# Performance work log

Measured on AMD Instinct MI355X. Metric: run time of the kernel, lower is better.

Reference implementation:

```python
import jax, jax.numpy as jnp
import numpy as np

STATE_DIM = 512
N_AGENTS = 16
N_ACTIONS = 32
EMBED = 512          # mixing_embed_dim
Q_IN = STATE_DIM + N_AGENTS * N_ACTIONS  # 1024 (coma_critic arch)
ROWS = 32768         # bs * ts = 64 * 512


def _linear_params(key, d_in, d_out):
    kw, kb = jax.random.split(key)
    bound = 1.0 / np.sqrt(d_in)
    W = jax.random.uniform(kw, (d_in, d_out), minval=-bound, maxval=bound, dtype=jnp.float32)
    b = jax.random.uniform(kb, (d_out,), minval=-bound, maxval=bound, dtype=jnp.float32)
    return W, b


def setup_inputs() -> dict:
    key = jax.random.key(0)
    ks = jax.random.split(key, 8)
    states = jax.random.normal(ks[0], (ROWS, STATE_DIM), dtype=jnp.float32)
    actions = jax.random.uniform(ks[1], (ROWS, N_AGENTS * N_ACTIONS), dtype=jnp.float32)
    Qw1, Qb1 = _linear_params(ks[2], Q_IN, EMBED)
    Qw2, Qb2 = _linear_params(ks[3], EMBED, EMBED)
    Qw3, Qb3 = _linear_params(ks[4], EMBED, 1)
    Vw1, Vb1 = _linear_params(ks[5], STATE_DIM, EMBED)
    Vw2, Vb2 = _linear_params(ks[6], EMBED, EMBED)
    Vw3, Vb3 = _linear_params(ks[7], EMBED, 1)
    return {
        "states": states, "actions": actions,
        "Qw1": Qw1, "Qb1": Qb1, "Qw2": Qw2, "Qb2": Qb2, "Qw3": Qw3, "Qb3": Qb3,
        "Vw1": Vw1, "Vb1": Vb1, "Vw2": Vw2, "Vb2": Vb2, "Vw3": Vw3, "Vb3": Vb3,
    }


def _mlp3(x, W1, b1, W2, b2, W3, b3):
    h = jax.nn.relu(x @ W1 + b1)
    h = jax.nn.relu(h @ W2 + b2)
    return h @ W3 + b3


def reference(states, actions,
              Qw1, Qb1, Qw2, Qb2, Qw3, Qb3,
              Vw1, Vb1, Vw2, Vb2, Vw3, Vb3):
    # coma_critic arch: inputs = cat([states, joint-action one-hots], dim=1)
    inputs = jnp.concatenate([states, actions], axis=1)  # [bs*ts, Q_IN]
    q_outputs = _mlp3(inputs, Qw1, Qb1, Qw2, Qb2, Qw3, Qb3)  # [bs*ts, 1]
    v_outputs = _mlp3(states, Vw1, Vb1, Vw2, Vb2, Vw3, Vb3)  # [bs*ts, 1]
    return q_outputs, v_outputs
```

## Files before the change

kernel.cpp:

```cpp
#include <hip/hip_runtime.h>


#define ROWS 32768
#define EMBED 512

using frag_ab = __attribute__((ext_vector_type(8))) short;
using f32x4   = __attribute__((ext_vector_type(4))) float;

__device__ __forceinline__ unsigned short f2bf(float f) {
    unsigned int u = __builtin_bit_cast(unsigned int, f);
    return (unsigned short)((u + 0x7fffu + ((u >> 16) & 1u)) >> 16);
}

__device__ __forceinline__ void async_copy16(const void* g, void* l) {
    __builtin_amdgcn_global_load_lds(
        (const __attribute__((address_space(1))) unsigned int*)g,
        (__attribute__((address_space(3))) unsigned int*)l, 16, 0, 0);
}

__global__ void init_out(float* __restrict__ out,
                         const float* __restrict__ qb3,
                         const float* __restrict__ vb3) {
    int i = blockIdx.x * 256 + threadIdx.x;
    out[i] = (i < ROWS) ? qb3[0] : vb3[0];
}

__global__ void convert_x(const float* __restrict__ states,
                          const float* __restrict__ actions,
                          unsigned short* __restrict__ X) {
    size_t t = (size_t)blockIdx.x * 256 + threadIdx.x;
    int m   = (int)(t >> 7);
    int col = (int)(t & 127) * 8;
    const float* src = (col < 512) ? states + (size_t)m * 512 + col
                                   : actions + (size_t)m * 512 + (col - 512);
    float4 a = *(const float4*)src;
    float4 b = *(const float4*)(src + 4);
    uint4 o;
    o.x = (unsigned)f2bf(a.x) | ((unsigned)f2bf(a.y) << 16);
    o.y = (unsigned)f2bf(a.z) | ((unsigned)f2bf(a.w) << 16);
    o.z = (unsigned)f2bf(b.x) | ((unsigned)f2bf(b.y) << 16);
    o.w = (unsigned)f2bf(b.z) | ((unsigned)f2bf(b.w) << 16);
    *(uint4*)(X + (size_t)m * 1024 + col) = o;
}

__global__ void prep_w(const float* __restrict__ Qw1, const float* __restrict__ Qw2,
                       const float* __restrict__ Vw1, const float* __restrict__ Vw2,
                       unsigned short* __restrict__ Qw1t, unsigned short* __restrict__ Qw2t,
                       unsigned short* __restrict__ Vw1t, unsigned short* __restrict__ Vw2t) {
    int t = blockIdx.x * 256 + threadIdx.x;
    if (t < 512 * 1024) {
        int n = t >> 10, k = t & 1023;
        Qw1t[t] = f2bf(Qw1[(size_t)k * 512 + n]);
    } else {
        t -= 512 * 1024;
        int seg = t >> 18;
        int r = t & 0x3ffff;
        int n = r >> 9, k = r & 511;
        const float* W = (seg == 0) ? Qw2 : (seg == 1) ? Vw1 : Vw2;
        unsigned short* O = (seg == 0) ? Qw2t : (seg == 1) ? Vw1t : Vw2t;
        O[r] = f2bf(W[(size_t)k * 512 + n]);
    }
}

template <bool FUSE>
__global__ __launch_bounds__(256, 2)
void gemm_bt(const unsigned short* __restrict__ A, int lda,
             const unsigned short* __restrict__ Wt, int K,
             const float* __restrict__ bias,
             unsigned short* __restrict__ H,
             const float* __restrict__ w3, float* __restrict__ out) {
    __shared__ __align__(16) unsigned short As[128 * 32];
    __shared__ __align__(16) unsigned short Bs[128 * 32];

    const int tid  = threadIdx.x;
    const int wave = tid >> 6, lane = tid & 63;
    const int bm = blockIdx.x * 128, bn = blockIdx.y * 128;
    const int wm = (wave & 1) * 64, wn = (wave >> 1) * 64;
    const int lrow = lane & 15, quad = lane >> 4;

    f32x4 acc[4][4] = {};

    const int lin  = wave * 1024 + lane * 16;
    const int rowS = lin >> 6;
    const int colS = (lin & 63) >> 1;

    const unsigned short* gA0 = A  + (size_t)(bm + rowS)      * lda + colS;
    const unsigned short* gA1 = A  + (size_t)(bm + rowS + 64) * lda + colS;
    const unsigned short* gB0 = Wt + (size_t)(bn + rowS)      * K   + colS;
    const unsigned short* gB1 = Wt + (size_t)(bn + rowS + 64) * K   + colS;
    unsigned short* ldsA0 = As + wave * 512;
    unsigned short* ldsA1 = As + 2048 + wave * 512;
    unsigned short* ldsB0 = Bs + wave * 512;
    unsigned short* ldsB1 = Bs + 2048 + wave * 512;

    for (int k0 = 0; k0 < K; k0 += 32) {
        async_copy16(gA0, ldsA0);
        async_copy16(gA1, ldsA1);
        async_copy16(gB0, ldsB0);
        async_copy16(gB1, ldsB1);
        gA0 += 32; gA1 += 32; gB0 += 32; gB1 += 32;
        __syncthreads();

        frag_ab af[4], bfr[4];
#pragma unroll
        for (int i = 0; i < 4; i++)
            af[i] = *(const frag_ab*)&As[(wm + i * 16 + lrow) * 32 + quad * 8];
#pragma unroll
        for (int j = 0; j < 4; j++)
            bfr[j] = *(const frag_ab*)&Bs[(wn + j * 16 + lrow) * 32 + quad * 8];
#pragma unroll
        for (int i = 0; i < 4; i++)
#pragma unroll
            for (int j = 0; j < 4; j++)
                acc[i][j] = __builtin_amdgcn_mfma_f32_16x16x32_bf16(
                    af[i], bfr[j], acc[i][j], 0, 0, 0);
        __syncthreads();
    }

    if (!FUSE) {
#pragma unroll
        for (int j = 0; j < 4; j++) {
            const int col = bn + wn + j * 16 + lrow;
            const float bc = bias[col];
#pragma unroll
            for (int i = 0; i < 4; i++) {
                const int row0 = bm + wm + i * 16 + quad * 4;
#pragma unroll
                for (int r = 0; r < 4; r++) {
                    float v = acc[i][j][r] + bc;
                    v = v > 0.0f ? v : 0.0f;
                    H[(size_t)(row0 + r) * EMBED + col] = f2bf(v);
                }
            }
        }
    } else {
        float bc[4], wc[4];
#pragma unroll
        for (int j = 0; j < 4; j++) {
            const int col = bn + wn + j * 16 + lrow;
            bc[j] = bias[col];
            wc[j] = w3[col];
        }
#pragma unroll
        for (int i = 0; i < 4; i++) {
#pragma unroll
            for (int r = 0; r < 4; r++) {
                float s = 0.0f;
#pragma unroll
                for (int j = 0; j < 4; j++) {
                    float v = acc[i][j][r] + bc[j];
                    v = v > 0.0f ? v : 0.0f;
                    s += v * wc[j];
                }
#pragma unroll
                for (int m = 1; m < 16; m <<= 1) s += __shfl_xor(s, m, 64);
                if (lrow == 0)
                    atomicAdd(&out[bm + wm + i * 16 + quad * 4 + r], s);
            }
        }
    }
}

extern "C" void kernel_launch(void* const* d_in, const int* in_sizes, int n_in,
                              void* d_out, int out_size, void* d_ws, size_t ws_size,
                              hipStream_t stream) {
    const float* states  = (const float*)d_in[0];
    const float* actions = (const float*)d_in[1];
    const float* Qw1 = (const float*)d_in[2];
    const float* Qb1 = (const float*)d_in[3];
    const float* Qw2 = (const float*)d_in[4];
    const float* Qb2 = (const float*)d_in[5];
    const float* Qw3 = (const float*)d_in[6];
    const float* Qb3 = (const float*)d_in[7];
    const float* Vw1 = (const float*)d_in[8];
    const float* Vb1 = (const float*)d_in[9];
    const float* Vw2 = (const float*)d_in[10];
    const float* Vb2 = (const float*)d_in[11];
    const float* Vw3 = (const float*)d_in[12];
    const float* Vb3 = (const float*)d_in[13];
    float* out = (float*)d_out;

    char* ws = (char*)d_ws;
    unsigned short* X    = (unsigned short*)ws;
    unsigned short* h1Q  = (unsigned short*)(ws + 67108864);
    unsigned short* h1V  = (unsigned short*)(ws + 100663296);
    unsigned short* Qw1t = (unsigned short*)(ws + 134217728);
    unsigned short* Qw2t = Qw1t + 512 * 1024;
    unsigned short* Vw1t = Qw2t + 512 * 512;
    unsigned short* Vw2t = Vw1t + 512 * 512;

    init_out<<<dim3(256), dim3(256), 0, stream>>>(out, Qb3, Vb3);
    convert_x<<<dim3(16384), dim3(256), 0, stream>>>(states, actions, X);
    prep_w<<<dim3(5120), dim3(256), 0, stream>>>(Qw1, Qw2, Vw1, Vw2,
                                                 Qw1t, Qw2t, Vw1t, Vw2t);

    dim3 grid(ROWS / 128, EMBED / 128);
    gemm_bt<false><<<grid, 256, 0, stream>>>(X, 1024, Qw1t, 1024, Qb1, h1Q, nullptr, nullptr);
    gemm_bt<false><<<grid, 256, 0, stream>>>(X, 1024, Vw1t, 512, Vb1, h1V, nullptr, nullptr);
    gemm_bt<true><<<grid, 256, 0, stream>>>(h1Q, 512, Qw2t, 512, Qb2, nullptr, Qw3, out);
    gemm_bt<true><<<grid, 256, 0, stream>>>(h1V, 512, Vw2t, 512, Vb2, nullptr, Vw3, out + ROWS);
}
```

Baseline: 294.2 us.

## Fuse fp32-to-bf16 input conversion into layer-1 GEMM and merge Q/V launches

Removes the separate convert_x pass by having layer1 load fp32 states/actions directly, truncate them to bf16 with a byte permute, and store them into padded LDS, with a register prefetch of the next K-slice. Q and V layer-1 GEMMs are merged into one launch, and so are the two layer-2 GEMMs, using blockIdx.x to select the branch. The grid is reordered so the N tiles of a row block are adjacent, which should improve L2 reuse of the A rows. This avoids writing and re-reading a 64MB bf16 intermediate but changes rounding from round-to-nearest-even to truncation, and the A loads now go through registers instead of async LDS copies.

New measurement: 352.0 us. 19.6% more time.

```diff
diff --git a/kernel.cpp b/kernel.cpp
--- a/kernel.cpp
+++ b/kernel.cpp
@@ -10,6 +10,11 @@
 __device__ __forceinline__ unsigned short f2bf(float f) {
     unsigned int u = __builtin_bit_cast(unsigned int, f);
     return (unsigned short)((u + 0x7fffu + ((u >> 16) & 1u)) >> 16);
+}
+
+__device__ __forceinline__ unsigned pk2(float lo, float hi) {
+    return __builtin_amdgcn_perm(__builtin_bit_cast(unsigned, hi),
+                                 __builtin_bit_cast(unsigned, lo), 0x07060302u);
 }
 
 __device__ __forceinline__ void async_copy16(const void* g, void* l) {
@@ -23,24 +28,6 @@
                          const float* __restrict__ vb3) {
     int i = blockIdx.x * 256 + threadIdx.x;
     out[i] = (i < ROWS) ? qb3[0] : vb3[0];
-}
-
-__global__ void convert_x(const float* __restrict__ states,
-                          const float* __restrict__ actions,
-                          unsigned short* __restrict__ X) {
-    size_t t = (size_t)blockIdx.x * 256 + threadIdx.x;
-    int m   = (int)(t >> 7);
-    int col = (int)(t & 127) * 8;
-    const float* src = (col < 512) ? states + (size_t)m * 512 + col
-                                   : actions + (size_t)m * 512 + (col - 512);
-    float4 a = *(const float4*)src;
-    float4 b = *(const float4*)(src + 4);
-    uint4 o;
-    o.x = (unsigned)f2bf(a.x) | ((unsigned)f2bf(a.y) << 16);
-    o.y = (unsigned)f2bf(a.z) | ((unsigned)f2bf(a.w) << 16);
-    o.z = (unsigned)f2bf(b.x) | ((unsigned)f2bf(b.y) << 16);
-    o.w = (unsigned)f2bf(b.z) | ((unsigned)f2bf(b.w) << 16);
-    *(uint4*)(X + (size_t)m * 1024 + col) = o;
 }
 
 __global__ void prep_w(const float* __restrict__ Qw1, const float* __restrict__ Qw2,
@@ -62,38 +49,133 @@
     }
 }
 
-template <bool FUSE>
-__global__ __launch_bounds__(256, 2)
-void gemm_bt(const unsigned short* __restrict__ A, int lda,
-             const unsigned short* __restrict__ Wt, int K,
-             const float* __restrict__ bias,
-             unsigned short* __restrict__ H,
-             const float* __restrict__ w3, float* __restrict__ out) {
+__global__ __launch_bounds__(256)
+void layer1(const float* __restrict__ states, const float* __restrict__ actions,
+            const unsigned short* __restrict__ Qw1t,
+            const unsigned short* __restrict__ Vw1t,
+            const float* __restrict__ Qb1, const float* __restrict__ Vb1,
+            unsigned short* __restrict__ h1Q, unsigned short* __restrict__ h1V) {
+    __shared__ __align__(16) unsigned short As[128 * 40];
+    __shared__ __align__(16) unsigned short Bs[128 * 32];
+
+    const int tid = threadIdx.x, wave = tid >> 6, lane = tid & 63;
+    const bool isV = blockIdx.x >= 4;
+    const int bn = (blockIdx.x & 3) * 128;
+    const int bm = blockIdx.y * 128;
+    const int K   = isV ? 512 : 1024;
+    const int ldb = isV ? 512 : 1024;
+    const unsigned short* Wt = isV ? Vw1t : Qw1t;
+    const float* bias = isV ? Vb1 : Qb1;
+    unsigned short* H = isV ? h1V : h1Q;
+
+    const int wm = (wave & 1) * 64, wn = (wave >> 1) * 64;
+    const int lrow = lane & 15, quad = lane >> 4;
+    f32x4 acc[4][4] = {};
+
+    const int lin  = wave * 1024 + lane * 16;
+    const int rowS = lin >> 6, colS = (lin & 63) >> 1;
+    const unsigned short* gB0 = Wt + (size_t)(bn + rowS)      * ldb + colS;
+    const unsigned short* gB1 = Wt + (size_t)(bn + rowS + 64) * ldb + colS;
+    unsigned short* ldsB0 = Bs + wave * 512;
+    unsigned short* ldsB1 = Bs + 2048 + wave * 512;
+
+    const int arow = tid >> 1, ahalf = tid & 1;
+    const size_t rowOff = (size_t)(bm + arow) * 512 + ahalf * 16;
+    unsigned short* wp = As + arow * 40 + ahalf * 16;
+
+    float4 f0, f1, f2, f3;
+    { const float4* g = (const float4*)(states + rowOff);
+      f0 = g[0]; f1 = g[1]; f2 = g[2]; f3 = g[3]; }
+
+    for (int k0 = 0; k0 < K; k0 += 32) {
+        async_copy16(gB0, ldsB0);
+        async_copy16(gB1, ldsB1);
+        gB0 += 32; gB1 += 32;
+        uint4 w0 = make_uint4(pk2(f0.x, f0.y), pk2(f0.z, f0.w),
+                              pk2(f1.x, f1.y), pk2(f1.z, f1.w));
+        uint4 w1 = make_uint4(pk2(f2.x, f2.y), pk2(f2.z, f2.w),
+                              pk2(f3.x, f3.y), pk2(f3.z, f3.w));
+        *(uint4*)wp       = w0;
+        *(uint4*)(wp + 8) = w1;
+        __syncthreads();
+
+        const int kn = k0 + 32;
+        if (kn < K) {
+            const float* Ab = (kn < 512) ? states : actions;
+            const float4* g = (const float4*)(Ab + rowOff + (kn & 511));
+            f0 = g[0]; f1 = g[1]; f2 = g[2]; f3 = g[3];
+        }
+
+        frag_ab af[4], bfr[4];
+#pragma unroll
+        for (int i = 0; i < 4; i++)
+            af[i] = *(const frag_ab*)&As[(wm + i * 16 + lrow) * 40 + quad * 8];
+#pragma unroll
+        for (int j = 0; j < 4; j++)
+            bfr[j] = *(const frag_ab*)&Bs[(wn + j * 16 + lrow) * 32 + quad * 8];
+#pragma unroll
+        for (int i = 0; i < 4; i++)
+#pragma unroll
+            for (int j = 0; j < 4; j++)
+                acc[i][j] = __builtin_amdgcn_mfma_f32_16x16x32_bf16(
+                    af[i], bfr[j], acc[i][j], 0, 0, 0);
+        __syncthreads();
+    }
+
+#pragma unroll
+    for (int j = 0; j < 4; j++) {
+        const int col = bn + wn + j * 16 + lrow;
+        const float bc = bias[col];
+#pragma unroll
+        for (int i = 0; i < 4; i++) {
+            const int row0 = bm + wm + i * 16 + quad * 4;
+#pragma unroll
+            for (int r = 0; r < 4; r++) {
+                float v = acc[i][j][r] + bc;
+                v = v > 0.0f ? v : 0.0f;
+                H[(size_t)(row0 + r) * EMBED + col] = f2bf(v);
+            }
+        }
+    }
+}
+
+__global__ __launch_bounds__(256)
+void layer2(const unsigned short* __restrict__ h1Q,
+            const unsigned short* __restrict__ h1V,
+            const unsigned short* __restrict__ Qw2t,
+            const unsigned short* __restrict__ Vw2t,
+            const float* __restrict__ Qb2, const float* __restrict__ Vb2,
+            const float* __restrict__ Qw3, const float* __restrict__ Vw3,
+            float* __restrict__ out) {
     __shared__ __align__(16) unsigned short As[128 * 32];
     __shared__ __align__(16) unsigned short Bs[128 * 32];
 
-    const int tid  = threadIdx.x;
-    const int wave = tid >> 6, lane = tid & 63;
-    const int bm = blockIdx.x * 128, bn = blockIdx.y * 128;
+    const int tid = threadIdx.x, wave = tid >> 6, lane = tid & 63;
+    const bool isV = blockIdx.x >= 4;
+    const int bn = (blockIdx.x & 3) * 128;
+    const int bm = blockIdx.y * 128;
+    const unsigned short* A  = isV ? h1V : h1Q;
+    const unsigned short* Wt = isV ? Vw2t : Qw2t;
+    const float* bias = isV ? Vb2 : Qb2;
+    const float* w3   = isV ? Vw3 : Qw3;
+    float* op = out + (isV ? ROWS : 0);
+
     const int wm = (wave & 1) * 64, wn = (wave >> 1) * 64;
     const int lrow = lane & 15, quad = lane >> 4;
-
     f32x4 acc[4][4] = {};
 
     const int lin  = wave * 1024 + lane * 16;
-    const int rowS = lin >> 6;
-    const int colS = (lin & 63) >> 1;
-
-    const unsigned short* gA0 = A  + (size_t)(bm + rowS)      * lda + colS;
-    const unsigned short* gA1 = A  + (size_t)(bm + rowS + 64) * lda + colS;
-    const unsigned short* gB0 = Wt + (size_t)(bn + rowS)      * K   + colS;
-    const unsigned short* gB1 = Wt + (size_t)(bn + rowS + 64) * K   + colS;
+    const int rowS = lin >> 6, colS = (lin & 63) >> 1;
+    const unsigned short* gA0 = A  + (size_t)(bm + rowS)      * 512 + colS;
+    const unsigned short* gA1 = A  + (size_t)(bm + rowS + 64) * 512 + colS;
+    const unsigned short* gB0 = Wt + (size_t)(bn + rowS)      * 512 + colS;
+    const unsigned short* gB1 = Wt + (size_t)(bn + rowS + 64) * 512 + colS;
     unsigned short* ldsA0 = As + wave * 512;
     unsigned short* ldsA1 = As + 2048 + wave * 512;
     unsigned short* ldsB0 = Bs + wave * 512;
     unsigned short* ldsB1 = Bs + 2048 + wave * 512;
 
-    for (int k0 = 0; k0 < K; k0 += 32) {
+    for (int k0 = 0; k0 < 512; k0 += 32) {
         async_copy16(gA0, ldsA0);
         async_copy16(gA1, ldsA1);
         async_copy16(gB0, ldsB0);
@@ -117,46 +199,28 @@
         __syncthreads();
     }
 
-    if (!FUSE) {
-#pragma unroll
-        for (int j = 0; j < 4; j++) {
-            const int col = bn + wn + j * 16 + lrow;
-            const float bc = bias[col];
-#pragma unroll
-            for (int i = 0; i < 4; i++) {
-                const int row0 = bm + wm + i * 16 + quad * 4;
-#pragma unroll
-                for (int r = 0; r < 4; r++) {
-                    float v = acc[i][j][r] + bc;
-                    v = v > 0.0f ? v : 0.0f;
-                    H[(size_t)(row0 + r) * EMBED + col] = f2bf(v);
-                }
+    float bc[4], wc[4];
+#pragma unroll
+    for (int j = 0; j < 4; j++) {
+        const int col = bn + wn + j * 16 + lrow;
+        bc[j] = bias[col];
+        wc[j] = w3[col];
+    }
+#pragma unroll
+    for (int i = 0; i < 4; i++) {
+#pragma unroll
+        for (int r = 0; r < 4; r++) {
+            float s = 0.0f;
+#pragma unroll
+            for (int j = 0; j < 4; j++) {
+                float v = acc[i][j][r] + bc[j];
+                v = v > 0.0f ? v : 0.0f;
+                s += v * wc[j];
             }
-        }
-    } else {
-        float bc[4], wc[4];
-#pragma unroll
-        for (int j = 0; j < 4; j++) {
-            const int col = bn + wn + j * 16 + lrow;
-            bc[j] = bias[col];
-            wc[j] = w3[col];
-        }
-#pragma unroll
-        for (int i = 0; i < 4; i++) {
-#pragma unroll
-            for (int r = 0; r < 4; r++) {
-                float s = 0.0f;
-#pragma unroll
-                for (int j = 0; j < 4; j++) {
-                    float v = acc[i][j][r] + bc[j];
-                    v = v > 0.0f ? v : 0.0f;
-                    s += v * wc[j];
-                }
-#pragma unroll
-                for (int m = 1; m < 16; m <<= 1) s += __shfl_xor(s, m, 64);
-                if (lrow == 0)
-                    atomicAdd(&out[bm + wm + i * 16 + quad * 4 + r], s);
-            }
+#pragma unroll
+            for (int m = 1; m < 16; m <<= 1) s += __shfl_xor(s, m, 64);
+            if (lrow == 0)
+                atomicAdd(&op[bm + wm + i * 16 + quad * 4 + r], s);
         }
     }
 }
@@ -181,22 +245,20 @@
     float* out = (float*)d_out;
 
     char* ws = (char*)d_ws;
-    unsigned short* X    = (unsigned short*)ws;
-    unsigned short* h1Q  = (unsigned short*)(ws + 67108864);
-    unsigned short* h1V  = (unsigned short*)(ws + 100663296);
-    unsigned short* Qw1t = (unsigned short*)(ws + 134217728);
+    unsigned short* h1Q  = (unsigned short*)ws;
+    unsigned short* h1V  = (unsigned short*)(ws + 33554432);
+    unsigned short* Qw1t = (unsigned short*)(ws + 67108864);
     unsigned short* Qw2t = Qw1t + 512 * 1024;
     unsigned short* Vw1t = Qw2t + 512 * 512;
     unsigned short* Vw2t = Vw1t + 512 * 512;
 
     init_out<<<dim3(256), dim3(256), 0, stream>>>(out, Qb3, Vb3);
-    convert_x<<<dim3(16384), dim3(256), 0, stream>>>(states, actions, X);
     prep_w<<<dim3(5120), dim3(256), 0, stream>>>(Qw1, Qw2, Vw1, Vw2,
                                                  Qw1t, Qw2t, Vw1t, Vw2t);
 
-    dim3 grid(ROWS / 128, EMBED / 128);
-    gemm_bt<false><<<grid, 256, 0, stream>>>(X, 1024, Qw1t, 1024, Qb1, h1Q, nullptr, nullptr);
-    gemm_bt<false><<<grid, 256, 0, stream>>>(X, 1024, Vw1t, 512, Vb1, h1V, nullptr, nullptr);
-    gemm_bt<true><<<grid, 256, 0, stream>>>(h1Q, 512, Qw2t, 512, Qb2, nullptr, Qw3, out);
-    gemm_bt<true><<<grid, 256, 0, stream>>>(h1V, 512, Vw2t, 512, Vb2, nullptr, Vw3, out + ROWS);
-}
+    dim3 grid(8, ROWS / 128);
+    layer1<<<grid, 256, 0, stream>>>(states, actions, Qw1t, Vw1t,
+                                     Qb1, Vb1, h1Q, h1V);
+    layer2<<<grid, 256, 0, stream>>>(h1Q, h1V, Qw2t, Vw2t,
+                                     Qb2, Vb2, Qw3, Vw3, out);
+}
```
